# Kernel optimization log

Measured on AMD Instinct MI355X. Metric: run time of the kernel, lower is better.

Reference implementation:

```python
import jax, jax.numpy as jnp
import numpy as np

H = 8          # num_heads
MAXP = 64      # max_temporal_length
EPS = 1e-5

def setup_inputs() -> dict:
    key = jax.random.key(0)
    ks = jax.random.split(key, 8)
    b, c, t, h, w = 2, 512, 16, 32, 32
    s = 0.02
    return {
        "x": jax.random.normal(ks[0], (b, c, t, h, w), jnp.float32),
        "ln_g": jnp.ones((c,), jnp.float32),
        "ln_b": jnp.zeros((c,), jnp.float32),
        "qkv_w": jax.random.normal(ks[1], (3 * c, c), jnp.float32) * s,
        "qkv_b": jax.random.normal(ks[2], (3 * c,), jnp.float32) * s,
        "k_table": jax.random.normal(ks[3], (2 * MAXP + 1, c // H), jnp.float32) * s,
        "v_table": jax.random.normal(ks[4], (2 * MAXP + 1, c // H), jnp.float32) * s,
        "proj_w": jax.random.normal(ks[5], (c, c), jnp.float32) * s,
        "proj_b": jax.random.normal(ks[6], (c,), jnp.float32) * s,
    }

def reference(x, ln_g, ln_b, qkv_w, qkv_b, k_table, v_table, proj_w, proj_b):
    b, c, t, h, w = x.shape
    ch = c // H
    B = b * h * w
    # (b c t h w) -> (b*h*w, t, c)
    seq = jnp.transpose(x, (0, 3, 4, 2, 1)).reshape(B, t, c)
    # LayerNorm
    mu = seq.mean(-1, keepdims=True)
    var = seq.var(-1, keepdims=True)
    nrm = (seq - mu) * jax.lax.rsqrt(var + EPS) * ln_g + ln_b
    # QKV projection: (B, t, 3c)
    qkv = nrm @ qkv_w.T + qkv_b
    q, k, v = jnp.split(qkv, 3, axis=-1)            # each (B, t, c)
    q = q.reshape(B, t, H, ch)
    k = k.reshape(B, t, H, ch)
    v = v.reshape(B, t, H, ch)
    # relative position lookup: (t, t, ch)
    idx = jnp.clip(jnp.arange(t)[None, :] - jnp.arange(t)[:, None], -MAXP, MAXP) + MAXP
    k_rp = k_table[idx]
    v_rp = v_table[idx]
    scale = 1.0 / math_sqrt_sqrt(ch)
    qs = q * scale
    # scores: content + relative-position key term
    weight = jnp.einsum('bqhc,bkhc->bhqk', qs, k * scale)
    weight = weight + jnp.einsum('bqhc,qkc->bhqk', qs, k_rp * scale)
    attn = jax.nn.softmax(weight, axis=-1)
    # values: content + relative-position value term
    a = jnp.einsum('bhqk,bkhc->bqhc', attn, v)
    a = a + jnp.einsum('bhqk,qkc->bqhc', attn, v_rp)
    a = a.reshape(B, t, c)
    out = a @ proj_w.T + proj_b                      # (B, t, c)
    out = out.reshape(b, h, w, t, c).transpose(0, 4, 3, 1, 2)
    return x + out

def math_sqrt_sqrt(ch):
    return float(np.sqrt(np.sqrt(ch)))
```

## Files before the change

kernel.cpp:

```cpp
#include <hip/hip_runtime.h>
#include <cstdint>
#include <cstddef>

#define Cc   512
#define Tt   16
#define HWn  1024
#define NBat 2
#define Mtot (NBat*Tt*HWn)
#define Hh   8
#define CHd  64
#define NQKV 1536

typedef _Float16 half8  __attribute__((ext_vector_type(8)));
typedef _Float16 half2t __attribute__((ext_vector_type(2)));
typedef float    f32x4  __attribute__((ext_vector_type(4)));

__device__ __forceinline__ void gl_lds16(const void* g, void* l) {
  __builtin_amdgcn_global_load_lds(
      (const __attribute__((address_space(1))) unsigned int*)g,
      (__attribute__((address_space(3))) unsigned int*)l, 16, 0, 0);
}

__device__ __forceinline__ float fdot2h(half2t a, half2t b, float c) {
#if __has_builtin(__builtin_amdgcn_fdot2)
  return __builtin_amdgcn_fdot2(a, b, c, false);
#else
  return c + (float)a[0] * (float)b[0] + (float)a[1] * (float)b[1];
#endif
}

__global__ __launch_bounds__(256) void wconv_k(const float* __restrict__ qw,
                                               const float* __restrict__ pw,
                                               _Float16* __restrict__ wq,
                                               _Float16* __restrict__ wp) {
  int i = blockIdx.x * 256 + threadIdx.x;
  if (i < NQKV * Cc) wq[i] = (_Float16)qw[i];
  if (i < Cc * Cc)   wp[i] = (_Float16)pw[i];
}

__global__ __launch_bounds__(256) void ln_k(const float* __restrict__ x,
                                            const float* __restrict__ g,
                                            const float* __restrict__ bln,
                                            _Float16* __restrict__ Ah) {
  int blk = blockIdx.x;
  int bi = blk >> 6, ti = (blk >> 2) & 15, hwc = blk & 3;
  int t = threadIdx.x;
  int hw = hwc * 256 + t;
  const float* xp = x + ((size_t)bi * Cc * Tt + ti) * HWn + hw;
  float s = 0.f, s2 = 0.f;
  #pragma unroll 8
  for (int ci = 0; ci < Cc; ++ci) {
    float v = xp[(size_t)ci * (Tt * HWn)];
    s += v; s2 += v * v;
  }
  float mean = s * (1.f / Cc);
  float var  = s2 * (1.f / Cc) - mean * mean;
  float rs   = rsqrtf(var + 1e-5f);
  size_t m = ((size_t)(bi * Tt + ti)) * HWn + hw;
  _Float16* dst = Ah + m * Cc;
  for (int k0 = 0; k0 < Cc; k0 += 8) {
    half8 hv;
    #pragma unroll
    for (int u = 0; u < 8; ++u) {
      int ci = k0 + u;
      float v = xp[(size_t)ci * (Tt * HWn)];
      hv[u] = (_Float16)((v - mean) * rs * g[ci] + bln[ci]);
    }
    *(half8*)(dst + k0) = hv;
  }
}

template<int NCOLS, bool PROJ>
__global__ __launch_bounds__(256) void gemm_k(const _Float16* __restrict__ A,
                                              const _Float16* __restrict__ W,
                                              const float* __restrict__ bias,
                                              _Float16* __restrict__ Cout,
                                              const float* __restrict__ xres,
                                              float* __restrict__ outF) {
  __shared__ union {
    struct { _Float16 A[3][128 * 32]; _Float16 B[3][128 * 32]; } s;
    float Cs[64 * 129];
  } u;

  const int tid  = threadIdx.x;
  const int wave = tid >> 6, lane = tid & 63;
  const int NTN = NCOLS / 128;
  const int tile_m = blockIdx.x / NTN;
  const int tile_n = blockIdx.x % NTN;
  const int m0 = tile_m * 128, n0 = tile_n * 128;
  const int wm = wave >> 1, wn = wave & 1;
  const int fr = lane & 15;
  const int fkc = lane >> 4;
  const int fsw = (fr >> 1) & 3;

  f32x4 acc[4][4] = {};

  const int srow_l = lane >> 2;
  const int schunk = lane & 3;

  auto stage = [&](int buf, int kt) {
    const int k0 = kt * 32;
    #pragma unroll
    for (int i = 0; i < 2; ++i) {
      int rowbase = i * 64 + wave * 16;
      int row = rowbase + srow_l;
      int cg = schunk ^ ((row >> 1) & 3);
      const _Float16* sa = A + (size_t)(m0 + row) * Cc + k0 + cg * 8;
      gl_lds16(sa, &u.s.A[buf][rowbase * 32]);
      const _Float16* sb = W + (size_t)(n0 + row) * Cc + k0 + cg * 8;
      gl_lds16(sb, &u.s.B[buf][rowbase * 32]);
    }
  };

  const int NK = Cc / 32;
  stage(0, 0);
  stage(1, 1);
  asm volatile("s_waitcnt vmcnt(4)" ::: "memory");
  __builtin_amdgcn_s_barrier();

  int bc = 0, b1 = 1, b2 = 2;
  for (int kt = 0; kt < NK; ++kt) {
    if (kt + 2 < NK) stage(b2, kt + 2);
    half8 af[4], bf[4];
    #pragma unroll
    for (int i = 0; i < 4; ++i) {
      int row = wm * 64 + i * 16 + fr;
      af[i] = *(const half8*)&u.s.A[bc][row * 32 + ((fkc ^ fsw) * 8)];
    }
    #pragma unroll
    for (int j = 0; j < 4; ++j) {
      int row = wn * 64 + j * 16 + fr;
      bf[j] = *(const half8*)&u.s.B[bc][row * 32 + ((fkc ^ fsw) * 8)];
    }
    #pragma unroll
    for (int i = 0; i < 4; ++i)
      #pragma unroll
      for (int j = 0; j < 4; ++j)
        acc[i][j] = __builtin_amdgcn_mfma_f32_16x16x32_f16(af[i], bf[j], acc[i][j], 0, 0, 0);
    if (kt < NK - 1) {
      if (kt + 2 < NK) asm volatile("s_waitcnt vmcnt(4)" ::: "memory");
      else             asm volatile("s_waitcnt vmcnt(0)" ::: "memory");
      __builtin_amdgcn_s_barrier();
    }
    int t0 = bc; bc = b1; b1 = b2; b2 = t0;
  }
  __syncthreads();

  const int bi_o = m0 >> 14, ti_o = (m0 >> 10) & 15, hw0 = m0 & 1023;
  #pragma unroll
  for (int r = 0; r < 2; ++r) {
    if (wm == r) {
      #pragma unroll
      for (int i = 0; i < 4; ++i)
        #pragma unroll
        for (int j = 0; j < 4; ++j)
          #pragma unroll
          for (int jj = 0; jj < 4; ++jj) {
            int row = i * 16 + (lane >> 4) * 4 + jj;
            int col = wn * 64 + j * 16 + (lane & 15);
            u.Cs[row * 129 + col] = acc[i][j][jj];
          }
    }
    __syncthreads();
    if (!PROJ) {
      for (int it = 0; it < 32; ++it) {
        int row = it * 2 + (tid >> 7);
        int col = tid & 127;
        float v = u.Cs[row * 129 + col] + bias[n0 + col];
        Cout[(size_t)(m0 + r * 64 + row) * NCOLS + n0 + col] = (_Float16)v;
      }
    } else {
      for (int it = 0; it < 32; ++it) {
        int col = it * 4 + (tid >> 6);
        int row = tid & 63;
        size_t oidx = (((size_t)(bi_o * Cc + n0 + col) * Tt) + ti_o) * HWn
                      + hw0 + r * 64 + row;
        outF[oidx] = u.Cs[row * 129 + col] + bias[n0 + col] + xres[oidx];
      }
    }
    __syncthreads();
  }
}

__global__ __launch_bounds__(256) void attn_k(const _Float16* __restrict__ qkv,
                                              const float* __restrict__ ktab,
                                              const float* __restrict__ vtab,
                                              _Float16* __restrict__ aout) {
  __shared__ alignas(16) _Float16 kt_s[31 * 72];
  __shared__ alignas(16) _Float16 vt_s[31 * 72];
  int bx = blockIdx.x;
  int bi = bx >> 9, h = (bx >> 6) & 7, hwc = bx & 63;
  int t = threadIdx.x;
  int qi = t >> 4, hwl = t & 15;
  int hw = hwc * 16 + hwl;

  for (int i = t; i < 31 * 64; i += 256) {
    int r = i >> 6, c = i & 63;
    kt_s[r * 72 + c] = (_Float16)ktab[(49 + r) * 64 + c];
    vt_s[r * 72 + c] = (_Float16)vtab[(49 + r) * 64 + c];
  }
  __syncthreads();

  size_t mq = ((size_t)(bi * Tt + qi)) * HWn + hw;
  size_t m0 = ((size_t)(bi * Tt + 0)) * HWn + hw;
  const size_t kstride = (size_t)HWn * NQKV;

  half8 qh[8];
  {
    const _Float16* qrow = qkv + mq * NQKV + h * CHd;
    #pragma unroll
    for (int u = 0; u < 8; ++u) qh[u] = ((const half8*)qrow)[u];
  }

  float s[16];
  {
    const _Float16* kp = qkv + m0 * NQKV + Cc + h * CHd;
    half8 kr[8], nx[8];
    #pragma unroll
    for (int u = 0; u < 8; ++u) kr[u] = ((const half8*)kp)[u];
    for (int ki = 0; ki < 16; ++ki) {
      const _Float16* knext = kp + kstride;
      if (ki < 15) {
        #pragma unroll
        for (int u = 0; u < 8; ++u) nx[u] = ((const half8*)knext)[u];
      }
      int d = ki - qi + 15;
      const _Float16* tp = &kt_s[d * 72];
      float a0 = 0.f, a1 = 0.f, a2 = 0.f, a3 = 0.f;
      #pragma unroll
      for (int u = 0; u < 8; ++u) {
        half8 tv = *(const half8*)(tp + u * 8);
        half8 sm = kr[u] + tv;
        const half2t* s2 = (const half2t*)&sm;
        const half2t* q2 = (const half2t*)&qh[u];
        a0 = fdot2h(q2[0], s2[0], a0);
        a1 = fdot2h(q2[1], s2[1], a1);
        a2 = fdot2h(q2[2], s2[2], a2);
        a3 = fdot2h(q2[3], s2[3], a3);
      }
      s[ki] = ((a0 + a1) + (a2 + a3)) * 0.125f;
      #pragma unroll
      for (int u = 0; u < 8; ++u) kr[u] = nx[u];
      kp = knext;
    }
  }

  float mx = s[0];
  #pragma unroll
  for (int ki = 1; ki < 16; ++ki) mx = fmaxf(mx, s[ki]);
  float sum = 0.f;
  #pragma unroll
  for (int ki = 0; ki < 16; ++ki) { s[ki] = __expf(s[ki] - mx); sum += s[ki]; }
  float inv = 1.f / sum;

  half8 o8[8];
  #pragma unroll
  for (int u = 0; u < 8; ++u) o8[u] = (half8)(_Float16)0.0f;
  {
    const _Float16* vp = qkv + m0 * NQKV + 2 * Cc + h * CHd;
    half8 vr[8], nx[8];
    #pragma unroll
    for (int u = 0; u < 8; ++u) vr[u] = ((const half8*)vp)[u];
    for (int ki = 0; ki < 16; ++ki) {
      const _Float16* vnext = vp + kstride;
      if (ki < 15) {
        #pragma unroll
        for (int u = 0; u < 8; ++u) nx[u] = ((const half8*)vnext)[u];
      }
      int d = ki - qi + 15;
      const _Float16* tp = &vt_s[d * 72];
      _Float16 ph = (_Float16)s[ki];
      half8 pk8;
      #pragma unroll
      for (int j = 0; j < 8; ++j) pk8[j] = ph;
      #pragma unroll
      for (int u = 0; u < 8; ++u) {
        half8 tv = *(const half8*)(tp + u * 8);
        half8 sm = vr[u] + tv;
        o8[u] += pk8 * sm;
      }
      #pragma unroll
      for (int u = 0; u < 8; ++u) vr[u] = nx[u];
      vp = vnext;
    }
  }

  _Float16* arow = aout + mq * Cc + h * CHd;
  #pragma unroll
  for (int u = 0; u < 8; ++u) {
    half8 hv;
    #pragma unroll
    for (int c = 0; c < 8; ++c) hv[c] = (_Float16)((float)o8[u][c] * inv);
    *(half8*)(arow + u * 8) = hv;
  }
}

extern "C" void kernel_launch(void* const* d_in, const int* in_sizes, int n_in,
                              void* d_out, int out_size, void* d_ws, size_t ws_size,
                              hipStream_t stream) {
  const float* x      = (const float*)d_in[0];
  const float* ln_g   = (const float*)d_in[1];
  const float* ln_b   = (const float*)d_in[2];
  const float* qkv_w  = (const float*)d_in[3];
  const float* qkv_b  = (const float*)d_in[4];
  const float* k_tab  = (const float*)d_in[5];
  const float* v_tab  = (const float*)d_in[6];
  const float* proj_w = (const float*)d_in[7];
  const float* proj_b = (const float*)d_in[8];
  float* out = (float*)d_out;

  _Float16* Ah   = (_Float16*)d_ws;
  _Float16* qkvb = Ah   + (size_t)Mtot * Cc;
  _Float16* ab   = qkvb + (size_t)Mtot * NQKV;
  _Float16* wq   = ab   + (size_t)Mtot * Cc;
  _Float16* wp   = wq   + (size_t)NQKV * Cc;

  wconv_k<<<3072, 256, 0, stream>>>(qkv_w, proj_w, wq, wp);
  ln_k<<<128, 256, 0, stream>>>(x, ln_g, ln_b, Ah);
  gemm_k<NQKV, false><<<(Mtot / 128) * (NQKV / 128), 256, 0, stream>>>(
      Ah, wq, qkv_b, qkvb, nullptr, nullptr);
  attn_k<<<1024, 256, 0, stream>>>(qkvb, k_tab, v_tab, ab);
  gemm_k<Cc, true><<<(Mtot / 128) * (Cc / 128), 256, 0, stream>>>(
      ab, wp, proj_b, nullptr, x, out);
}
```

Baseline: 497.4 us.

## Stage K and V tiles in LDS and share them across query threads

The attention kernel previously had each of the 16 query threads per spatial position reload all 16 K and V rows from global memory. Now each thread loads one K row into shared memory and holds one V row in registers. After the score phase the V rows are written into the same LDS buffer, so global K/V traffic drops about 16x. The cost is a larger LDS footprint (about 45KB per block), which may limit occupancy, plus extra barriers and a possible LDS bank conflict risk.

Result: faster. 408.5 us (-17.9%).

```diff
diff --git a/kernel.cpp b/kernel.cpp
--- a/kernel.cpp
+++ b/kernel.cpp
@@ -186,63 +186,62 @@
                                               const float* __restrict__ ktab,
                                               const float* __restrict__ vtab,
                                               _Float16* __restrict__ aout) {
-  __shared__ alignas(16) _Float16 kt_s[31 * 72];
-  __shared__ alignas(16) _Float16 vt_s[31 * 72];
-  int bx = blockIdx.x;
-  int bi = bx >> 9, h = (bx >> 6) & 7, hwc = bx & 63;
-  int t = threadIdx.x;
-  int qi = t >> 4, hwl = t & 15;
-  int hw = hwc * 16 + hwl;
+  __shared__ _Float16 kv_s[16 * 16 * 72];
+  __shared__ _Float16 kt_s[31 * 72];
+  __shared__ _Float16 vt_s[31 * 72];
+
+  const int bx = blockIdx.x;
+  const int bi = bx >> 9, h = (bx >> 6) & 7, hwc = bx & 63;
+  const int t = threadIdx.x;
+  const int qi = t >> 4, hwl = t & 15;
+  const int hw = hwc * 16 + hwl;
 
   for (int i = t; i < 31 * 64; i += 256) {
     int r = i >> 6, c = i & 63;
     kt_s[r * 72 + c] = (_Float16)ktab[(49 + r) * 64 + c];
     vt_s[r * 72 + c] = (_Float16)vtab[(49 + r) * 64 + c];
   }
+
+  const int ski = t >> 4, shl = t & 15;
+  const _Float16* ksrc = qkv + (((size_t)(bi * Tt + ski)) * HWn + hwc * 16 + shl) * NQKV
+                         + Cc + h * CHd;
+  _Float16* kdst = &kv_s[(ski * 16 + shl) * 72];
+  #pragma unroll
+  for (int u = 0; u < 8; ++u)
+    *(half8*)(kdst + u * 8) = ((const half8*)ksrc)[u];
+
+  const _Float16* vsrc = ksrc + Cc;
+  half8 vreg[8];
+  #pragma unroll
+  for (int u = 0; u < 8; ++u) vreg[u] = ((const half8*)vsrc)[u];
+
+  size_t mq = ((size_t)(bi * Tt + qi)) * HWn + hw;
+  const _Float16* qrow = qkv + mq * NQKV + h * CHd;
+  half8 qh[8];
+  #pragma unroll
+  for (int u = 0; u < 8; ++u) qh[u] = ((const half8*)qrow)[u];
+
   __syncthreads();
 
-  size_t mq = ((size_t)(bi * Tt + qi)) * HWn + hw;
-  size_t m0 = ((size_t)(bi * Tt + 0)) * HWn + hw;
-  const size_t kstride = (size_t)HWn * NQKV;
-
-  half8 qh[8];
-  {
-    const _Float16* qrow = qkv + mq * NQKV + h * CHd;
-    #pragma unroll
-    for (int u = 0; u < 8; ++u) qh[u] = ((const half8*)qrow)[u];
-  }
-
   float s[16];
-  {
-    const _Float16* kp = qkv + m0 * NQKV + Cc + h * CHd;
-    half8 kr[8], nx[8];
-    #pragma unroll
-    for (int u = 0; u < 8; ++u) kr[u] = ((const half8*)kp)[u];
-    for (int ki = 0; ki < 16; ++ki) {
-      const _Float16* knext = kp + kstride;
-      if (ki < 15) {
-        #pragma unroll
-        for (int u = 0; u < 8; ++u) nx[u] = ((const half8*)knext)[u];
-      }
-      int d = ki - qi + 15;
-      const _Float16* tp = &kt_s[d * 72];
-      float a0 = 0.f, a1 = 0.f, a2 = 0.f, a3 = 0.f;
-      #pragma unroll
-      for (int u = 0; u < 8; ++u) {
-        half8 tv = *(const half8*)(tp + u * 8);
-        half8 sm = kr[u] + tv;
-        const half2t* s2 = (const half2t*)&sm;
-        const half2t* q2 = (const half2t*)&qh[u];
-        a0 = fdot2h(q2[0], s2[0], a0);
-        a1 = fdot2h(q2[1], s2[1], a1);
-        a2 = fdot2h(q2[2], s2[2], a2);
-        a3 = fdot2h(q2[3], s2[3], a3);
-      }
-      s[ki] = ((a0 + a1) + (a2 + a3)) * 0.125f;
-      #pragma unroll
-      for (int u = 0; u < 8; ++u) kr[u] = nx[u];
-      kp = knext;
-    }
+  for (int ki = 0; ki < 16; ++ki) {
+    int d = ki - qi + 15;
+    const _Float16* kp = &kv_s[(ki * 16 + hwl) * 72];
+    const _Float16* tp = &kt_s[d * 72];
+    float a0 = 0.f, a1 = 0.f, a2 = 0.f, a3 = 0.f;
+    #pragma unroll
+    for (int u = 0; u < 8; ++u) {
+      half8 kvv = *(const half8*)(kp + u * 8);
+      half8 tv  = *(const half8*)(tp + u * 8);
+      half8 sm  = kvv + tv;
+      const half2t* s2 = (const half2t*)&sm;
+      const half2t* q2 = (const half2t*)&qh[u];
+      a0 = fdot2h(q2[0], s2[0], a0);
+      a1 = fdot2h(q2[1], s2[1], a1);
+      a2 = fdot2h(q2[2], s2[2], a2);
+      a3 = fdot2h(q2[3], s2[3], a3);
+    }
+    s[ki] = ((a0 + a1) + (a2 + a3)) * 0.125f;
   }
 
   float mx = s[0];
@@ -253,35 +252,30 @@
   for (int ki = 0; ki < 16; ++ki) { s[ki] = __expf(s[ki] - mx); sum += s[ki]; }
   float inv = 1.f / sum;
 
+  __syncthreads();
+
+  #pragma unroll
+  for (int u = 0; u < 8; ++u)
+    *(half8*)(kdst + u * 8) = vreg[u];
+  __syncthreads();
+
   half8 o8[8];
   #pragma unroll
   for (int u = 0; u < 8; ++u) o8[u] = (half8)(_Float16)0.0f;
-  {
-    const _Float16* vp = qkv + m0 * NQKV + 2 * Cc + h * CHd;
-    half8 vr[8], nx[8];
-    #pragma unroll
-    for (int u = 0; u < 8; ++u) vr[u] = ((const half8*)vp)[u];
-    for (int ki = 0; ki < 16; ++ki) {
-      const _Float16* vnext = vp + kstride;
-      if (ki < 15) {
-        #pragma unroll
-        for (int u = 0; u < 8; ++u) nx[u] = ((const half8*)vnext)[u];
-      }
-      int d = ki - qi + 15;
-      const _Float16* tp = &vt_s[d * 72];
-      _Float16 ph = (_Float16)s[ki];
-      half8 pk8;
-      #pragma unroll
-      for (int j = 0; j < 8; ++j) pk8[j] = ph;
-      #pragma unroll
-      for (int u = 0; u < 8; ++u) {
-        half8 tv = *(const half8*)(tp + u * 8);
-        half8 sm = vr[u] + tv;
-        o8[u] += pk8 * sm;
-      }
-      #pragma unroll
-      for (int u = 0; u < 8; ++u) vr[u] = nx[u];
-      vp = vnext;
+  for (int ki = 0; ki < 16; ++ki) {
+    int d = ki - qi + 15;
+    const _Float16* vp = &kv_s[(ki * 16 + hwl) * 72];
+    const _Float16* tp = &vt_s[d * 72];
+    _Float16 ph = (_Float16)s[ki];
+    half8 pk8;
+    #pragma unroll
+    for (int j = 0; j < 8; ++j) pk8[j] = ph;
+    #pragma unroll
+    for (int u = 0; u < 8; ++u) {
+      half8 vr = *(const half8*)(vp + u * 8);
+      half8 tv = *(const half8*)(tp + u * 8);
+      half8 sm = vr + tv;
+      o8[u] += pk8 * sm;
     }
   }
 
```
